# Kernel tuning notes

Measured on AMD Instinct MI355X. Metric: run time of the kernel, lower is better.

## Reference

```python
import jax, jax.numpy as jnp
import numpy as np

REPR_OUT = (16, 16, 16)   # multiplicities for l=0,1,2
STRIDE = 2                # GatedBlock stride with smooth_stride=True -> low-pass+stride after gate
PAD = 2                   # conv padding
C_IN = 72                 # 8*1 + 8*3 + 8*5
C_OUT_GATED = 176         # 144 fields + 32 gate scalars
KSIZE = 5


def conv3d(x, w, stride, padding):
    return jax.lax.conv_general_dilated(
        x, w, window_strides=(stride,) * 3,
        padding=[(padding, padding)] * 3,
        dimension_numbers=('NCDHW', 'OIDHW', 'NCDHW'))


def low_pass_filter(z, scale, stride):
    # gaussian blur (sigma from scale) applied depthwise, then strided -- as in se3cnn
    sigma = 0.5 * (scale ** 2 - 1) ** 0.5
    size = int(1 + 2 * 2.5 * sigma)
    if size % 2 == 0:
        size += 1
    r = np.arange(size) - size // 2
    g1 = np.exp(-r.astype(np.float64) ** 2 / (2 * sigma ** 2))
    g = g1[:, None, None] * g1[None, :, None] * g1[None, None, :]
    g = (g / g.sum()).astype(np.float32)
    B, C = z.shape[0], z.shape[1]
    zz = z.reshape(B * C, 1, *z.shape[2:])
    out = conv3d(zz, jnp.asarray(g)[None, None], stride, size // 2)
    return out.reshape(B, C, *out.shape[2:])


def gate(y, scalar_bias, gate_bias):
    # y: [B, 176, X, Y, Z]; split into 144 field channels + 32 gate scalars
    size_out = sum(mul * (2 * n + 1) for n, mul in enumerate(REPR_OUT))
    B, _, nx, ny, nz = y.shape
    g = jax.nn.sigmoid(y[:, size_out:] + gate_bias[None, :, None, None, None])
    fields = []
    begin_y, begin_g = 0, 0
    for n, mul in enumerate(REPR_OUT):
        if mul == 0:
            continue
        dim = 2 * n + 1
        fy = y[:, begin_y:begin_y + mul * dim]
        if n == 0:
            # scalar fields: bias + relu (ScalarActivation)
            fields.append(jax.nn.relu(fy + scalar_bias[None, :, None, None, None]))
        else:
            fg = g[:, begin_g:begin_g + mul]
            begin_g += mul
            f = fy.reshape(B, mul, dim, nx, ny, nz) * fg[:, :, None]  # broadcast gate over 2l+1
            fields.append(f.reshape(B, mul * dim, nx, ny, nz))
        begin_y += mul * dim
    return jnp.concatenate(fields, axis=1)  # [B, 144, X, Y, Z]


def setup_inputs() -> dict:
    key = jax.random.key(0)
    k1, k2, k3, k4 = jax.random.split(key, 4)
    fan_in = C_IN * KSIZE ** 3
    x = jax.random.normal(k1, (4, C_IN, 32, 32, 32), dtype=jnp.float32)
    W = jax.random.normal(k2, (C_OUT_GATED, C_IN, KSIZE, KSIZE, KSIZE), dtype=jnp.float32) / np.sqrt(fan_in)
    scalar_bias = jax.random.normal(k3, (REPR_OUT[0],), dtype=jnp.float32) * 0.1
    gate_bias = jax.random.normal(k4, (sum(REPR_OUT[1:]),), dtype=jnp.float32) * 0.1
    return {'x': x, 'W': W, 'scalar_bias': scalar_bias, 'gate_bias': gate_bias}


def reference(x, W, scalar_bias, gate_bias):
    y = conv3d(x, W, 1, PAD)                 # SE3 conv at stride 1 (smooth_stride)
    z = gate(y, scalar_bias, gate_bias)      # per-irrep gated nonlinearity
    z = low_pass_filter(z, STRIDE, STRIDE)   # gaussian low-pass + stride 2
    return z
```

## Files before the change

kernel.cpp:

```cpp
#include <hip/hip_runtime.h>
#include <cstdint>
#include <cstddef>

typedef short short8 __attribute__((ext_vector_type(8)));
typedef float floatx4 __attribute__((ext_vector_type(4)));
typedef unsigned short u16;

__device__ __forceinline__ u16 f2bf(float f) {
    unsigned u = __float_as_uint(f);
    u += 0x7FFFu + ((u >> 16) & 1u);
    return (u16)(u >> 16);
}
__device__ __forceinline__ float bf2f(u16 h) {
    return __uint_as_float(((unsigned)h) << 16);
}

__device__ __forceinline__ void gload_lds16(const u16* g, u16* l) {
    __builtin_amdgcn_global_load_lds(
        (const __attribute__((address_space(1))) void*)g,
        (__attribute__((address_space(3))) void*)l, 16, 0, 0);
}

__global__ __launch_bounds__(256) void k_transpose_x(const float* __restrict__ x,
                                                     u16* __restrict__ xt) {
    __shared__ float tile[72 * 33];
    const int bx = blockIdx.x;
    const int tid = threadIdx.x;
    const int b = bx >> 10, d = (bx >> 5) & 31, h = bx & 31;
    const float* src = x + (size_t)b * 72 * 32768 + d * 1024 + h * 32;
    for (int e = tid; e < 2304; e += 256) {
        int ci = e >> 5, w = e & 31;
        tile[ci * 33 + w] = src[(size_t)ci * 32768 + w];
    }
    __syncthreads();
    u16* dst = xt + (size_t)bx * 2304;
    for (int e = tid; e < 2304; e += 256) {
        int w = e / 72, ci = e - w * 72;
        dst[e] = f2bf(tile[ci * 33 + w]);
    }
}

__global__ __launch_bounds__(256) void k_prep_w(const float* __restrict__ W,
                                                u16* __restrict__ wt) {
    const int gid = blockIdx.x * 256 + threadIdx.x;
    const int frag = gid >> 6, lane = gid & 63;
    const int nb = frag % 11;
    int t = frag / 11;
    const int kb = t % 12;
    t = t / 12;
    const int kh = t % 5, kd = t / 5;
    const int n = lane & 15, q8 = (lane >> 4) * 8;
    const int co = nb * 16 + n;
    u16 v[8] __attribute__((aligned(16)));
    #pragma unroll
    for (int j = 0; j < 8; ++j) {
        int k = kb * 32 + q8 + j;
        u16 r = 0;
        if (k < 360) {
            int kw = k / 72, ci = k - kw * 72;
            r = f2bf(W[((size_t)co * 72 + ci) * 125 + kd * 25 + kh * 5 + kw]);
        }
        v[j] = r;
    }
    *(uint4*)(wt + (size_t)gid * 8) = *(const uint4*)v;
}

#define LP 2592
#define MFMA_BF16 __builtin_amdgcn_mfma_f32_16x16x32_bf16

template<int CB>
__device__ __forceinline__ void conv_body(const u16* __restrict__ xt,
                                          const u16* __restrict__ wt,
                                          const float* __restrict__ scalar_bias,
                                          const float* __restrict__ gate_bias,
                                          u16* __restrict__ zt,
                                          u16* sx, u16* sB,
                                          int b, int d, int h0,
                                          int tid, int lane, int wv,
                                          int c15, int q) {
    constexpr int NF = CB ? 6 : 5;

    floatx4 acc[4][NF];
    #pragma unroll
    for (int i = 0; i < 4; ++i) {
        #pragma unroll
        for (int j = 0; j < NF; ++j) acc[i][j] = (floatx4){0.f, 0.f, 0.f, 0.f};
    }

    const int laneA = c15 * 72 + q * 8;

    for (int kd = 0; kd < 5; ++kd) {
        const int dp = d + kd - 2;
        if (dp < 0 || dp >= 32) continue;
        const u16* wt_kd = wt + (size_t)kd * 5 * 67584;

        const u16* srcbase = xt + (size_t)((b * 32 + dp) * 32) * 2304;
        for (int idx = tid; idx < 12 * 324; idx += 256) {
            int r = idx / 324, c = idx - r * 324;
            int hp = h0 + r - 2;
            uint4 val = make_uint4(0u, 0u, 0u, 0u);
            if (hp >= 0 && hp < 32 && c >= 18 && c < 306)
                val = *(const uint4*)(srcbase + (size_t)hp * 2304 + (c * 8 - 144));
            *(uint4*)(&sx[r * LP + c * 8]) = val;
        }

        auto stage = [&](int kk, int s) {
            #pragma unroll
            for (int t = 0; t < 2; ++t) {
                const int f = wv + t * 4;
                if (f < NF) {
                    const int nb = CB ? ((f == 5) ? 10 : (f + 4))
                                      : ((f == 4) ? 9 : f);
                    gload_lds16(wt_kd + (size_t)kk * 5632 + nb * 512 + lane * 8,
                                sB + s * 3072 + f * 512);
                }
            }
        };

        stage(0, 0);
        stage(1, 1);
        __syncthreads();

        int kh = 0, kb = 0, s0 = 0;
        #pragma unroll 1
        for (int kk = 0; kk < 60; ++kk) {
            int s2 = s0 + 2; if (s2 >= 3) s2 -= 3;
            if (kk < 58) stage(kk + 2, s2);
            const u16* ap = sx + (2 * wv + kh) * LP + laneA + kb * 32;
            short8 A0 = *(const short8*)(ap);
            short8 A1 = *(const short8*)(ap + 1152);
            short8 A2 = *(const short8*)(ap + LP);
            short8 A3 = *(const short8*)(ap + LP + 1152);
            const u16* bb = sB + s0 * 3072 + lane * 8;
            __builtin_amdgcn_s_setprio(1);
            #pragma unroll
            for (int f = 0; f < NF; ++f) {
                short8 bv = *(const short8*)(bb + f * 512);
                acc[0][f] = MFMA_BF16(A0, bv, acc[0][f], 0, 0, 0);
                acc[1][f] = MFMA_BF16(A1, bv, acc[1][f], 0, 0, 0);
                acc[2][f] = MFMA_BF16(A2, bv, acc[2][f], 0, 0, 0);
                acc[3][f] = MFMA_BF16(A3, bv, acc[3][f], 0, 0, 0);
            }
            __builtin_amdgcn_s_setprio(0);
            __syncthreads();
            if (++kb == 12) { kb = 0; ++kh; }
            if (++s0 == 3) s0 = 0;
        }
    }

    constexpr int GF = NF - 1;
    constexpr int NGATED = CB ? 5 : 3;
    int   slA[NGATED];
    float gbA[NGATED];
    #pragma unroll
    for (int j = 0; j < NGATED; ++j) {
        const int nb = CB ? (j + 4) : (j + 1);
        const int idx = (nb - 1) * 16 + c15;
        const int mul = (nb <= 3) ? (idx / 3) : (16 + (idx - 48) / 5);
        slA[j] = (lane & 48) | (mul & 15);
        gbA[j] = gate_bias[mul];
    }
    const float sb = CB ? 0.f : scalar_bias[c15];
    #pragma unroll
    for (int mi = 0; mi < 4; ++mi) {
        const int hl = 2 * wv + (mi >> 1);
        const int wh = mi & 1;
        const size_t zrow0 = (size_t)((b * 32 + d) * 32 + (h0 + hl)) * 32;
        #pragma unroll
        for (int r = 0; r < 4; ++r) {
            const int w = wh * 16 + q * 4 + r;
            u16* zp = zt + (zrow0 + w) * 144;
            const float gv = acc[mi][GF][r];
            if (CB == 0)
                zp[c15] = f2bf(fmaxf(acc[mi][0][r] + sb, 0.f));
            #pragma unroll
            for (int j = 0; j < NGATED; ++j) {
                const int nb = CB ? (j + 4) : (j + 1);
                float ys = __shfl(gv, slA[j], 64);
                float g  = 1.f / (1.f + __expf(-(ys + gbA[j])));
                zp[nb * 16 + c15] = f2bf(acc[mi][CB ? j : (j + 1)][r] * g);
            }
        }
    }
}

__global__ __launch_bounds__(256, 2) void k_conv(const u16* __restrict__ xt,
                                                 const u16* __restrict__ wt,
                                                 const float* __restrict__ scalar_bias,
                                                 const float* __restrict__ gate_bias,
                                                 u16* __restrict__ zt) {
    __shared__ __align__(16) u16 sx[12 * LP];
    __shared__ __align__(16) u16 sB[3 * 3072];
    const int bx = blockIdx.x;
    const int swz = (bx & 7) * 128 + (bx >> 3);
    const int cb = swz & 1, ht = (swz >> 1) & 3, d = (swz >> 3) & 31, b = swz >> 8;
    const int h0 = ht * 8;
    const int tid = threadIdx.x, lane = tid & 63, wv = tid >> 6;
    const int c15 = lane & 15, q = lane >> 4;

    if (cb == 0)
        conv_body<0>(xt, wt, scalar_bias, gate_bias, zt, sx, sB, b, d, h0, tid, lane, wv, c15, q);
    else
        conv_body<1>(xt, wt, scalar_bias, gate_bias, zt, sx, sB, b, d, h0, tid, lane, wv, c15, q);
}

__global__ __launch_bounds__(256) void k_lowpass(const u16* __restrict__ zt,
                                                 float* __restrict__ out) {
    const int gid = blockIdx.x * 256 + threadIdx.x;
    const int row = gid / 288;
    const int it  = gid - row * 288;
    const int c8 = it >> 4, ow = it & 15;
    const int oh = row & 15, od = (row >> 4) & 15, b = row >> 8;
    const float lw[5] = {0.03208210f, 0.23705644f, 0.46172277f, 0.23705644f, 0.03208210f};
    float a[8];
    #pragma unroll
    for (int j = 0; j < 8; ++j) a[j] = 0.f;
    for (int kd = 0; kd < 5; ++kd) {
        const int dz = 2 * od + kd - 2;
        if (dz < 0 || dz >= 32) continue;
        for (int kh = 0; kh < 5; ++kh) {
            const int hz = 2 * oh + kh - 2;
            if (hz < 0 || hz >= 32) continue;
            const float whd = lw[kd] * lw[kh];
            const u16* base = zt + (size_t)((b * 32 + dz) * 32 + hz) * 32 * 144 + c8 * 8;
            #pragma unroll
            for (int kw = 0; kw < 5; ++kw) {
                const int wz = 2 * ow + kw - 2;
                if (wz < 0 || wz >= 32) continue;
                const float wt3 = whd * lw[kw];
                u16 v[8] __attribute__((aligned(16)));
                *(uint4*)v = *(const uint4*)(base + (size_t)wz * 144);
                #pragma unroll
                for (int j = 0; j < 8; ++j) a[j] += wt3 * bf2f(v[j]);
            }
        }
    }
    const int c0 = c8 * 8;
    float* op = out + ((size_t)b * 144 + c0) * 4096 + od * 256 + oh * 16 + ow;
    #pragma unroll
    for (int j = 0; j < 8; ++j) op[(size_t)j * 4096] = a[j];
}

extern "C" void kernel_launch(void* const* d_in, const int* in_sizes, int n_in,
                              void* d_out, int out_size, void* d_ws, size_t ws_size,
                              hipStream_t stream) {
    const float* x  = (const float*)d_in[0];
    const float* W  = (const float*)d_in[1];
    const float* sb = (const float*)d_in[2];
    const float* gb = (const float*)d_in[3];
    float* out = (float*)d_out;

    char* ws = (char*)d_ws;
    u16* xt = (u16*)(ws);
    u16* wt = (u16*)(ws + 18874368);
    u16* zt = (u16*)(ws + 22253568);

    hipLaunchKernelGGL(k_transpose_x, dim3(4096), dim3(256), 0, stream, x, xt);
    hipLaunchKernelGGL(k_prep_w,      dim3(825),  dim3(256), 0, stream, W, wt);
    hipLaunchKernelGGL(k_conv,        dim3(1024), dim3(256), 0, stream, xt, wt, sb, gb, zt);
    hipLaunchKernelGGL(k_lowpass,     dim3(1152), dim3(256), 0, stream, zt, out);
}
```

Baseline: 570.9 us.

## Register-prefetch conv weights instead of LDS staging; split low-pass into separable passes

The conv kernel no longer stages weight tiles into LDS with async global-to-LDS loads and a per-step barrier. Each wave now loads its B fragments straight from global memory into a three-deep rotating set of registers, so the inner loop needs no __syncthreads. The LDS row pitch grows slightly, likely to reduce bank conflicts on A reads. The 3D Gaussian low-pass is split into an H/W pass that writes an fp32 intermediate, reusing the xt workspace, and a separate D pass. In exchange this costs more VGPRs, which may hurt occupancy, plus redundant global weight reads per wave and an extra kernel launch and intermediate round trip.

```diff
diff --git a/kernel.cpp b/kernel.cpp
--- a/kernel.cpp
+++ b/kernel.cpp
@@ -13,12 +13,6 @@
 }
 __device__ __forceinline__ float bf2f(u16 h) {
     return __uint_as_float(((unsigned)h) << 16);
-}
-
-__device__ __forceinline__ void gload_lds16(const u16* g, u16* l) {
-    __builtin_amdgcn_global_load_lds(
-        (const __attribute__((address_space(1))) void*)g,
-        (__attribute__((address_space(3))) void*)l, 16, 0, 0);
 }
 
 __global__ __launch_bounds__(256) void k_transpose_x(const float* __restrict__ x,
@@ -65,7 +59,7 @@
     *(uint4*)(wt + (size_t)gid * 8) = *(const uint4*)v;
 }
 
-#define LP 2592
+#define LP 2624
 #define MFMA_BF16 __builtin_amdgcn_mfma_f32_16x16x32_bf16
 
 template<int CB>
@@ -74,7 +68,7 @@
                                           const float* __restrict__ scalar_bias,
                                           const float* __restrict__ gate_bias,
                                           u16* __restrict__ zt,
-                                          u16* sx, u16* sB,
+                                          u16* sx,
                                           int b, int d, int h0,
                                           int tid, int lane, int wv,
                                           int c15, int q) {
@@ -88,63 +82,59 @@
     }
 
     const int laneA = c15 * 72 + q * 8;
+    short8 B0[NF], B1[NF], B2[NF];
 
     for (int kd = 0; kd < 5; ++kd) {
         const int dp = d + kd - 2;
         if (dp < 0 || dp >= 32) continue;
         const u16* wt_kd = wt + (size_t)kd * 5 * 67584;
 
+        __syncthreads();
         const u16* srcbase = xt + (size_t)((b * 32 + dp) * 32) * 2304;
-        for (int idx = tid; idx < 12 * 324; idx += 256) {
-            int r = idx / 324, c = idx - r * 324;
+        for (int idx = tid; idx < 12 * 328; idx += 256) {
+            int r = idx / 328, c = idx - r * 328;
             int hp = h0 + r - 2;
             uint4 val = make_uint4(0u, 0u, 0u, 0u);
             if (hp >= 0 && hp < 32 && c >= 18 && c < 306)
                 val = *(const uint4*)(srcbase + (size_t)hp * 2304 + (c * 8 - 144));
             *(uint4*)(&sx[r * LP + c * 8]) = val;
         }
-
-        auto stage = [&](int kk, int s) {
-            #pragma unroll
-            for (int t = 0; t < 2; ++t) {
-                const int f = wv + t * 4;
-                if (f < NF) {
-                    const int nb = CB ? ((f == 5) ? 10 : (f + 4))
-                                      : ((f == 4) ? 9 : f);
-                    gload_lds16(wt_kd + (size_t)kk * 5632 + nb * 512 + lane * 8,
-                                sB + s * 3072 + f * 512);
-                }
+        __syncthreads();
+
+        auto bload = [&](short8 (&B)[NF], int kkn) {
+            const u16* gp = wt_kd + (size_t)kkn * 5632 + lane * 8;
+            #pragma unroll
+            for (int f = 0; f < NF; ++f) {
+                const int nb = CB ? ((f == 5) ? 10 : (f + 4)) : ((f == 4) ? 9 : f);
+                B[f] = *(const short8*)(gp + nb * 512);
             }
         };
 
-        stage(0, 0);
-        stage(1, 1);
-        __syncthreads();
-
-        int kh = 0, kb = 0, s0 = 0;
-        #pragma unroll 1
-        for (int kk = 0; kk < 60; ++kk) {
-            int s2 = s0 + 2; if (s2 >= 3) s2 -= 3;
-            if (kk < 58) stage(kk + 2, s2);
+        int kh = 0, kb = 0;
+        auto cstep = [&](short8 (&Bc)[NF], short8 (&Bn)[NF], int kkn) {
+            bload(Bn, kkn);
             const u16* ap = sx + (2 * wv + kh) * LP + laneA + kb * 32;
             short8 A0 = *(const short8*)(ap);
             short8 A1 = *(const short8*)(ap + 1152);
             short8 A2 = *(const short8*)(ap + LP);
             short8 A3 = *(const short8*)(ap + LP + 1152);
-            const u16* bb = sB + s0 * 3072 + lane * 8;
-            __builtin_amdgcn_s_setprio(1);
             #pragma unroll
             for (int f = 0; f < NF; ++f) {
-                short8 bv = *(const short8*)(bb + f * 512);
-                acc[0][f] = MFMA_BF16(A0, bv, acc[0][f], 0, 0, 0);
-                acc[1][f] = MFMA_BF16(A1, bv, acc[1][f], 0, 0, 0);
-                acc[2][f] = MFMA_BF16(A2, bv, acc[2][f], 0, 0, 0);
-                acc[3][f] = MFMA_BF16(A3, bv, acc[3][f], 0, 0, 0);
+                acc[0][f] = MFMA_BF16(A0, Bc[f], acc[0][f], 0, 0, 0);
+                acc[1][f] = MFMA_BF16(A1, Bc[f], acc[1][f], 0, 0, 0);
+                acc[2][f] = MFMA_BF16(A2, Bc[f], acc[2][f], 0, 0, 0);
+                acc[3][f] = MFMA_BF16(A3, Bc[f], acc[3][f], 0, 0, 0);
             }
-            __builtin_amdgcn_s_setprio(0);
-            __syncthreads();
             if (++kb == 12) { kb = 0; ++kh; }
-            if (++s0 == 3) s0 = 0;
+        };
+
+        bload(B0, 0);
+        bload(B1, 1);
+        #pragma unroll 1
+        for (int kk = 0; kk < 60; kk += 3) {
+            cstep(B0, B2, kk + 2 < 60 ? kk + 2 : 59);
+            cstep(B1, B0, kk + 3 < 60 ? kk + 3 : 59);
+            cstep(B2, B1, kk + 4 < 60 ? kk + 4 : 59);
         }
     }
 
@@ -190,7 +180,6 @@
                                                  const float* __restrict__ gate_bias,
                                                  u16* __restrict__ zt) {
     __shared__ __align__(16) u16 sx[12 * LP];
-    __shared__ __align__(16) u16 sB[3 * 3072];
     const int bx = blockIdx.x;
     const int swz = (bx & 7) * 128 + (bx >> 3);
     const int cb = swz & 1, ht = (swz >> 1) & 3, d = (swz >> 3) & 31, b = swz >> 8;
@@ -199,46 +188,68 @@
     const int c15 = lane & 15, q = lane >> 4;
 
     if (cb == 0)
-        conv_body<0>(xt, wt, scalar_bias, gate_bias, zt, sx, sB, b, d, h0, tid, lane, wv, c15, q);
+        conv_body<0>(xt, wt, scalar_bias, gate_bias, zt, sx, b, d, h0, tid, lane, wv, c15, q);
     else
-        conv_body<1>(xt, wt, scalar_bias, gate_bias, zt, sx, sB, b, d, h0, tid, lane, wv, c15, q);
-}
-
-__global__ __launch_bounds__(256) void k_lowpass(const u16* __restrict__ zt,
-                                                 float* __restrict__ out) {
+        conv_body<1>(xt, wt, scalar_bias, gate_bias, zt, sx, b, d, h0, tid, lane, wv, c15, q);
+}
+
+__global__ __launch_bounds__(256) void k_lowpass_wh(const u16* __restrict__ zt,
+                                                    float* __restrict__ tmp) {
     const int gid = blockIdx.x * 256 + threadIdx.x;
-    const int row = gid / 288;
-    const int it  = gid - row * 288;
-    const int c8 = it >> 4, ow = it & 15;
-    const int oh = row & 15, od = (row >> 4) & 15, b = row >> 8;
+    const int c8 = gid % 18;
+    int r = gid / 18;
+    const int ow = r & 15; r >>= 4;
+    const int oh = r & 15; r >>= 4;
+    const int d = r & 31;
+    const int b = r >> 5;
     const float lw[5] = {0.03208210f, 0.23705644f, 0.46172277f, 0.23705644f, 0.03208210f};
     float a[8];
     #pragma unroll
     for (int j = 0; j < 8; ++j) a[j] = 0.f;
+    const u16* zb = zt + (size_t)((b * 32 + d) * 32) * 32 * 144 + c8 * 8;
+    for (int kh = 0; kh < 5; ++kh) {
+        const int hz = 2 * oh + kh - 2;
+        if (hz < 0 || hz >= 32) continue;
+        const u16* rowp = zb + (size_t)hz * 32 * 144;
+        #pragma unroll
+        for (int kw = 0; kw < 5; ++kw) {
+            const int wz = 2 * ow + kw - 2;
+            if (wz < 0 || wz >= 32) continue;
+            const float wt2 = lw[kh] * lw[kw];
+            u16 v[8] __attribute__((aligned(16)));
+            *(uint4*)v = *(const uint4*)(rowp + (size_t)wz * 144);
+            #pragma unroll
+            for (int j = 0; j < 8; ++j) a[j] += wt2 * bf2f(v[j]);
+        }
+    }
+    float* tp = tmp + (size_t)(((b * 32 + d) * 16 + oh) * 16 + ow) * 144 + c8 * 8;
+    *(float4*)(tp)     = make_float4(a[0], a[1], a[2], a[3]);
+    *(float4*)(tp + 4) = make_float4(a[4], a[5], a[6], a[7]);
+}
+
+__global__ __launch_bounds__(256) void k_lowpass_d(const float* __restrict__ tmp,
+                                                   float* __restrict__ out) {
+    const int gid = blockIdx.x * 256 + threadIdx.x;
+    const int oh = gid & 15;
+    int r = gid >> 4;
+    const int od = r & 15; r >>= 4;
+    const int c = r % 144;
+    const int b = r / 144;
+    const float lw[5] = {0.03208210f, 0.23705644f, 0.46172277f, 0.23705644f, 0.03208210f};
+    float a[16];
+    #pragma unroll
+    for (int j = 0; j < 16; ++j) a[j] = 0.f;
     for (int kd = 0; kd < 5; ++kd) {
         const int dz = 2 * od + kd - 2;
         if (dz < 0 || dz >= 32) continue;
-        for (int kh = 0; kh < 5; ++kh) {
-            const int hz = 2 * oh + kh - 2;
-            if (hz < 0 || hz >= 32) continue;
-            const float whd = lw[kd] * lw[kh];
-            const u16* base = zt + (size_t)((b * 32 + dz) * 32 + hz) * 32 * 144 + c8 * 8;
-            #pragma unroll
-            for (int kw = 0; kw < 5; ++kw) {
-                const int wz = 2 * ow + kw - 2;
-                if (wz < 0 || wz >= 32) continue;
-                const float wt3 = whd * lw[kw];
-                u16 v[8] __attribute__((aligned(16)));
-                *(uint4*)v = *(const uint4*)(base + (size_t)wz * 144);
-                #pragma unroll
-                for (int j = 0; j < 8; ++j) a[j] += wt3 * bf2f(v[j]);
-            }
-        }
-    }
-    const int c0 = c8 * 8;
-    float* op = out + ((size_t)b * 144 + c0) * 4096 + od * 256 + oh * 16 + ow;
-    #pragma unroll
-    for (int j = 0; j < 8; ++j) op[(size_t)j * 4096] = a[j];
+        const float w = lw[kd];
+        const float* base = tmp + (size_t)(((b * 32 + dz) * 16 + oh) * 16) * 144 + c;
+        #pragma unroll
+        for (int ow = 0; ow < 16; ++ow) a[ow] += w * base[(size_t)ow * 144];
+    }
+    float* op = out + ((size_t)(b * 144 + c) * 4096) + od * 256 + oh * 16;
+    #pragma unroll
+    for (int ow = 0; ow < 16; ++ow) op[ow] = a[ow];
 }
 
 extern "C" void kernel_launch(void* const* d_in, const int* in_sizes, int n_in,
@@ -254,9 +265,11 @@
     u16* xt = (u16*)(ws);
     u16* wt = (u16*)(ws + 18874368);
     u16* zt = (u16*)(ws + 22253568);
+    float* tmp = (float*)(ws);
 
     hipLaunchKernelGGL(k_transpose_x, dim3(4096), dim3(256), 0, stream, x, xt);
     hipLaunchKernelGGL(k_prep_w,      dim3(825),  dim3(256), 0, stream, W, wt);
     hipLaunchKernelGGL(k_conv,        dim3(1024), dim3(256), 0, stream, xt, wt, sb, gb, zt);
-    hipLaunchKernelGGL(k_lowpass,     dim3(1152), dim3(256), 0, stream, zt, out);
-}
+    hipLaunchKernelGGL(k_lowpass_wh,  dim3(2304), dim3(256), 0, stream, zt, tmp);
+    hipLaunchKernelGGL(k_lowpass_d,   dim3(576),  dim3(256), 0, stream, tmp, out);
+}
```

Result: slower. 613.6 us (+7.5%).
